# Kernel tuning notes

Hardware: AMD Instinct MI355X
Metric: run time of the kernel (lower is better)

Reference implementation:

```python
import jax, jax.numpy as jnp
import numpy as np

D = 64          # node_hidden_dim
MP_STEPS = 6    # num_step_message_passing
S2S_STEPS = 6   # num_step_set2set
LSTM_LAYERS = 3 # num_layer_set2set


def setup_inputs() -> dict:
    key = jax.random.key(0)
    ks = jax.random.split(key, 32)
    N, E, B = 10000, 50000, 500
    node_in, edge_in, edge_hid, out_dim = 15, 5, 128, 12
    s = 0.1
    inp = {}
    inp["node_feat"] = jax.random.normal(ks[0], (N, node_in), jnp.float32)
    inp["edge_feat"] = jax.random.normal(ks[1], (E, edge_in), jnp.float32)
    inp["src"] = jax.random.randint(ks[2], (E,), 0, N)
    inp["dst"] = jax.random.randint(ks[3], (E,), 0, N)
    inp["graph_ids"] = jnp.sort(jax.random.randint(ks[4], (N,), 0, B))
    inp["num_graphs"] = B
    # lin0
    inp["lin0_W"] = jax.random.normal(ks[5], (node_in, D), jnp.float32) * s
    inp["lin0_b"] = jnp.zeros((D,), jnp.float32)
    # edge network MLP (Linear -> ReLU -> Linear), output reshaped to D x D per edge
    inp["em_W1"] = jax.random.normal(ks[6], (edge_in, edge_hid), jnp.float32) * s
    inp["em_b1"] = jnp.zeros((edge_hid,), jnp.float32)
    inp["em_W2"] = jax.random.normal(ks[7], (edge_hid, D * D), jnp.float32) * 0.02
    inp["em_b2"] = jnp.zeros((D * D,), jnp.float32)
    inp["conv_bias"] = jnp.zeros((D,), jnp.float32)
    # GRU (input D, hidden D), torch layout: [3*D, in], gate order r,z,n
    inp["gru_Wih"] = jax.random.normal(ks[8], (3 * D, D), jnp.float32) * s
    inp["gru_Whh"] = jax.random.normal(ks[9], (3 * D, D), jnp.float32) * s
    inp["gru_bih"] = jnp.zeros((3 * D,), jnp.float32)
    inp["gru_bhh"] = jnp.zeros((3 * D,), jnp.float32)
    # Set2Set LSTM: input 2*D, hidden D, 3 layers. torch layout [4*D, in], gates i,f,g,o
    inp["lstm0_Wih"] = jax.random.normal(ks[10], (4 * D, 2 * D), jnp.float32) * s
    inp["lstm0_Whh"] = jax.random.normal(ks[11], (4 * D, D), jnp.float32) * s
    inp["lstm0_bih"] = jnp.zeros((4 * D,), jnp.float32)
    inp["lstm0_bhh"] = jnp.zeros((4 * D,), jnp.float32)
    inp["lstm12_Wih"] = jax.random.normal(ks[12], (2, 4 * D, D), jnp.float32) * s
    inp["lstm12_Whh"] = jax.random.normal(ks[13], (2, 4 * D, D), jnp.float32) * s
    inp["lstm12_bih"] = jnp.zeros((2, 4 * D), jnp.float32)
    inp["lstm12_bhh"] = jnp.zeros((2, 4 * D), jnp.float32)
    # output head
    inp["lin1_W"] = jax.random.normal(ks[14], (2 * D, D), jnp.float32) * s
    inp["lin1_b"] = jnp.zeros((D,), jnp.float32)
    inp["lin2_W"] = jax.random.normal(ks[15], (D, out_dim), jnp.float32) * s
    inp["lin2_b"] = jnp.zeros((out_dim,), jnp.float32)
    return inp


def _mpnn(node_feat, edge_feat, src, dst, graph_ids, num_graphs,
          lin0_W, lin0_b, em_W1, em_b1, em_W2, em_b2, conv_bias,
          gru_Wih, gru_Whh, gru_bih, gru_bhh,
          lstm0_Wih, lstm0_Whh, lstm0_bih, lstm0_bhh,
          lstm12_Wih, lstm12_Whh, lstm12_bih, lstm12_bhh,
          lin1_W, lin1_b, lin2_W, lin2_b):
    N = node_feat.shape[0]
    E = edge_feat.shape[0]
    B = num_graphs
    # initial node embedding
    out = jax.nn.relu(node_feat @ lin0_W + lin0_b)      # [N, D]
    h = out                                             # GRU hidden (seq_len=1, 1 layer)
    # per-edge weight matrices (edge features are static across steps)
    We = (jax.nn.relu(edge_feat @ em_W1 + em_b1) @ em_W2 + em_b2).reshape(E, D, D)
    for _ in range(MP_STEPS):
        # NNConv: gather src -> per-edge matvec -> scatter-add to dst
        msg = jnp.einsum('ei,eio->eo', out[src], We)    # [E, D]
        agg = jax.ops.segment_sum(msg, dst, num_segments=N) + conv_bias
        m = jax.nn.relu(agg)                            # [N, D]
        # GRU cell (torch gate order r, z, n)
        gx = m @ gru_Wih.T + gru_bih
        gh = h @ gru_Whh.T + gru_bhh
        rx, zx, nx = jnp.split(gx, 3, axis=-1)
        rh, zh, nh = jnp.split(gh, 3, axis=-1)
        r = jax.nn.sigmoid(rx + rh)
        z = jax.nn.sigmoid(zx + zh)
        n = jnp.tanh(nx + r * nh)
        h = (1.0 - z) * n + z * h
        out = h
    # Set2Set readout: 3-layer LSTM over steps, attention over nodes per graph
    h_l = [jnp.zeros((B, D), out.dtype) for _ in range(LSTM_LAYERS)]
    c_l = [jnp.zeros((B, D), out.dtype) for _ in range(LSTM_LAYERS)]
    q_star = jnp.zeros((B, 2 * D), out.dtype)
    for _ in range(S2S_STEPS):
        x = q_star
        for l in range(LSTM_LAYERS):
            if l == 0:
                Wih, Whh, bih, bhh = lstm0_Wih, lstm0_Whh, lstm0_bih, lstm0_bhh
            else:
                Wih, Whh = lstm12_Wih[l - 1], lstm12_Whh[l - 1]
                bih, bhh = lstm12_bih[l - 1], lstm12_bhh[l - 1]
            g = x @ Wih.T + bih + h_l[l] @ Whh.T + bhh
            i_g, f_g, g_g, o_g = jnp.split(g, 4, axis=-1)
            c_l[l] = jax.nn.sigmoid(f_g) * c_l[l] + jax.nn.sigmoid(i_g) * jnp.tanh(g_g)
            h_l[l] = jax.nn.sigmoid(o_g) * jnp.tanh(c_l[l])
            x = h_l[l]
        q = x                                           # [B, D]
        # segment softmax attention
        e = jnp.sum(out * q[graph_ids], axis=-1)        # [N]
        emax = jax.ops.segment_max(e, graph_ids, num_segments=B)
        ex = jnp.exp(e - emax[graph_ids])
        denom = jax.ops.segment_sum(ex, graph_ids, num_segments=B)
        alpha = ex / denom[graph_ids]                   # [N]
        readout = jax.ops.segment_sum(alpha[:, None] * out, graph_ids, num_segments=B)
        q_star = jnp.concatenate([q, readout], axis=-1) # [B, 2D]
    y = jax.nn.relu(q_star @ lin1_W + lin1_b) @ lin2_W + lin2_b
    return y


def reference(node_feat, edge_feat, src, dst, graph_ids, num_graphs,
              lin0_W, lin0_b, em_W1, em_b1, em_W2, em_b2, conv_bias,
              gru_Wih, gru_Whh, gru_bih, gru_bhh,
              lstm0_Wih, lstm0_Whh, lstm0_bih, lstm0_bhh,
              lstm12_Wih, lstm12_Whh, lstm12_bih, lstm12_bhh,
              lin1_W, lin1_b, lin2_W, lin2_b):
    return _mpnn(node_feat, edge_feat, src, dst, graph_ids, num_graphs,
                 lin0_W, lin0_b, em_W1, em_b1, em_W2, em_b2, conv_bias,
                 gru_Wih, gru_Whh, gru_bih, gru_bhh,
                 lstm0_Wih, lstm0_Whh, lstm0_bih, lstm0_bhh,
                 lstm12_Wih, lstm12_Whh, lstm12_bih, lstm12_bhh,
                 lin1_W, lin1_b, lin2_W, lin2_b)
```

## Files before the change

### kernel.cpp

```cpp
#include <hip/hip_runtime.h>
#include <math.h>

#define NGRAPH 500
#define MP_STEPS 6
#define S2S_STEPS 6
#define S2S_CAP 128

typedef _Float16 h8 __attribute__((ext_vector_type(8)));
typedef float f4 __attribute__((ext_vector_type(4)));

__device__ __forceinline__ float sigmoidf_(float v){ return 1.0f/(1.0f + expf(-v)); }

__global__ void k_zero(float* __restrict__ p, int n){
  int i = blockIdx.x*256 + threadIdx.x;
  if(i < n) p[i] = 0.f;
}

__global__ void k_lin0(const float* __restrict__ nf, const float* __restrict__ W,
                       const float* __restrict__ b, float* __restrict__ x, int N){
  int n = blockIdx.x*4 + (threadIdx.x >> 6);
  int d = threadIdx.x & 63;
  if(n >= N) return;
  float acc = b[d];
#pragma unroll
  for(int i=0;i<15;i++) acc = fmaf(nf[n*15+i], W[i*64+d], acc);
  x[n*64+d] = fmaxf(acc, 0.0f);
}

__global__ void k_edgeh(const float* __restrict__ ef, const float* __restrict__ W1,
                        const float* __restrict__ b1, _Float16* __restrict__ he, int E){
  int e = blockIdx.x;
  int h = threadIdx.x;
  if(e >= E || h >= 160) return;
  float v;
  if(h < 128){
    float acc = b1[h];
#pragma unroll
    for(int i=0;i<5;i++) acc = fmaf(ef[e*5+i], W1[i*128+h], acc);
    v = fmaxf(acc, 0.f);
  } else {
    v = (h == 128) ? 1.0f : 0.0f;
  }
  he[(size_t)e*160 + h] = (_Float16)v;
}

__global__ void k_prepW2(const float* __restrict__ W2, const float* __restrict__ b2,
                         _Float16* __restrict__ W2T){
  int idx = blockIdx.x*256 + threadIdx.x;
  if(idx >= 4096*160) return;
  int n = idx / 160, k = idx % 160;
  float v = (k < 128) ? W2[(size_t)k*4096 + n] : ((k == 128) ? b2[n] : 0.f);
  W2T[idx] = (_Float16)v;
}

__global__ __launch_bounds__(512, 2) void k_fmsg(
    const _Float16* __restrict__ he,
    const _Float16* __restrict__ W2T,
    const float* __restrict__ x,
    const int* __restrict__ src, const int* __restrict__ dst,
    float* __restrict__ agg, int E)
{
  __shared__ _Float16 hs[128*160];
  __shared__ float xsT[64*132];
  __shared__ int ds_dst[128];
  const int tid  = threadIdx.x;
  const int wave = tid >> 6;
  const int mrow = wave >> 2;
  const int cg   = wave & 3;
  const int lane = tid & 63;
  const int quad = lane >> 4;
  const int l15  = lane & 15;
  const int e0   = blockIdx.x * 128;

  for(int t = tid; t < 2560; t += 512){
    int r = t / 20, c = t % 20;
    uint4 v = make_uint4(0,0,0,0);
    if(e0 + r < E) v = *(const uint4*)&he[(size_t)(e0+r)*160 + c*8];
    *(uint4*)&hs[r*160 + c*8] = v;
  }
  {
    int j = tid >> 2, qc = tid & 3;
    int sj = (e0 + j < E) ? src[e0 + j] : 0;
    const float4* xr = (const float4*)(x + (size_t)sj*64);
#pragma unroll
    for(int k=0;k<4;k++){
      float4 v = xr[qc*4 + k];
      int ib = qc*16 + k*4;
      xsT[(ib+0)*132 + j] = v.x;
      xsT[(ib+1)*132 + j] = v.y;
      xsT[(ib+2)*132 + j] = v.z;
      xsT[(ib+3)*132 + j] = v.w;
    }
  }
  if(tid < 128) ds_dst[tid] = (e0 + tid < E) ? dst[e0 + tid] : 0;
  __syncthreads();

  h8 af[4][5];
#pragma unroll
  for(int mt=0;mt<4;mt++)
#pragma unroll
    for(int ks=0;ks<5;ks++)
      af[mt][ks] = *(const h8*)&hs[(mrow*64 + mt*16 + l15)*160 + ks*32 + (quad<<3)];

  const _Float16* bbase = W2T + ((size_t)(cg*16 + l15))*160 + (quad<<3);
  h8 bf[5], bn[5];
#pragma unroll
  for(int ks=0;ks<5;ks++) bf[ks] = *(const h8*)(bbase + ks*32);

  f4 macc[4];
#pragma unroll
  for(int mt=0;mt<4;mt++) macc[mt] = (f4){0.f,0.f,0.f,0.f};

#pragma unroll 2
  for(int i=0;i<64;i++){
    if(i < 63){
      const _Float16* nb = bbase + (size_t)(i+1)*64*160;
#pragma unroll
      for(int ks=0;ks<5;ks++) bn[ks] = *(const h8*)(nb + ks*32);
    }
    f4 g0 = (f4){0.f,0.f,0.f,0.f}, g1 = g0, g2 = g0, g3 = g0;
#pragma unroll
    for(int ks=0;ks<5;ks++){
      g0 = __builtin_amdgcn_mfma_f32_16x16x32_f16(af[0][ks], bf[ks], g0, 0, 0, 0);
      g1 = __builtin_amdgcn_mfma_f32_16x16x32_f16(af[1][ks], bf[ks], g1, 0, 0, 0);
      g2 = __builtin_amdgcn_mfma_f32_16x16x32_f16(af[2][ks], bf[ks], g2, 0, 0, 0);
      g3 = __builtin_amdgcn_mfma_f32_16x16x32_f16(af[3][ks], bf[ks], g3, 0, 0, 0);
    }
    f4 xs0 = *(const f4*)&xsT[i*132 + mrow*64 + (quad<<2) +  0];
    f4 xs1 = *(const f4*)&xsT[i*132 + mrow*64 + (quad<<2) + 16];
    f4 xs2 = *(const f4*)&xsT[i*132 + mrow*64 + (quad<<2) + 32];
    f4 xs3 = *(const f4*)&xsT[i*132 + mrow*64 + (quad<<2) + 48];
    macc[0] += xs0 * g0;
    macc[1] += xs1 * g1;
    macc[2] += xs2 * g2;
    macc[3] += xs3 * g3;
#pragma unroll
    for(int ks=0;ks<5;ks++) bf[ks] = bn[ks];
  }

  const int col = cg*16 + l15;
#pragma unroll
  for(int mt=0;mt<4;mt++){
#pragma unroll
    for(int r=0;r<4;r++){
      int edge = mrow*64 + mt*16 + (quad<<2) + r;
      if(e0 + edge < E)
        atomicAdd(&agg[(size_t)ds_dst[edge]*64 + col], macc[mt][r]);
    }
  }
}

__global__ __launch_bounds__(256) void k_gru2(
    float* __restrict__ x, float* __restrict__ agg, const float* __restrict__ cb,
    const float* __restrict__ WihT, const float* __restrict__ WhhT,
    const float* __restrict__ bih, const float* __restrict__ bhh, int N)
{
  __shared__ float ms[32*64], hs2[32*64];
  const int tid = threadIdx.x;
  const int n0 = blockIdx.x*32;
  for(int t=tid; t<2048; t+=256){
    int n = n0 + (t>>6), d = t&63;
    float mv=0.f, hv=0.f;
    if(n < N){
      mv = fmaxf(agg[(size_t)n*64+d] + cb[d], 0.f);
      agg[(size_t)n*64+d] = 0.f;
      hv = x[(size_t)n*64+d];
    }
    ms[t]=mv; hs2[t]=hv;
  }
  __syncthreads();
  const int gx = tid & 31, ng = tid >> 5;
  float ar[4][2]={{0}}, az[4][2]={{0}}, anx[4][2]={{0}}, anh[4][2]={{0}};
#pragma unroll 4
  for(int k=0;k<64;k++){
    float wi0=WihT[k*192+gx],     wi1=WihT[k*192+gx+32];
    float wi2=WihT[k*192+gx+64],  wi3=WihT[k*192+gx+96];
    float wi4=WihT[k*192+gx+128], wi5=WihT[k*192+gx+160];
    float wh0=WhhT[k*192+gx],     wh1=WhhT[k*192+gx+32];
    float wh2=WhhT[k*192+gx+64],  wh3=WhhT[k*192+gx+96];
    float wh4=WhhT[k*192+gx+128], wh5=WhhT[k*192+gx+160];
#pragma unroll
    for(int j=0;j<4;j++){
      float mk = ms[(ng*4+j)*64+k], hk = hs2[(ng*4+j)*64+k];
      ar[j][0] = fmaf(mk,wi0, fmaf(hk,wh0, ar[j][0]));
      ar[j][1] = fmaf(mk,wi1, fmaf(hk,wh1, ar[j][1]));
      az[j][0] = fmaf(mk,wi2, fmaf(hk,wh2, az[j][0]));
      az[j][1] = fmaf(mk,wi3, fmaf(hk,wh3, az[j][1]));
      anx[j][0]= fmaf(mk,wi4, anx[j][0]);
      anx[j][1]= fmaf(mk,wi5, anx[j][1]);
      anh[j][0]= fmaf(hk,wh4, anh[j][0]);
      anh[j][1]= fmaf(hk,wh5, anh[j][1]);
    }
  }
#pragma unroll
  for(int j=0;j<4;j++){
    int n = n0 + ng*4 + j;
    if(n >= N) continue;
#pragma unroll
    for(int c=0;c<2;c++){
      int d = gx + 32*c;
      float r  = sigmoidf_(ar[j][c] + bih[d]     + bhh[d]);
      float z  = sigmoidf_(az[j][c] + bih[64+d]  + bhh[64+d]);
      float nn = tanhf(anx[j][c] + bih[128+d] + r*(anh[j][c] + bhh[128+d]));
      float hv = hs2[(ng*4+j)*64+d];
      x[(size_t)n*64+d] = (1.f - z)*nn + z*hv;
    }
  }
}

__global__ void k_tr_gru(const float* __restrict__ Wih, const float* __restrict__ Whh,
                         float* __restrict__ WihT, float* __restrict__ WhhT){
  int idx = blockIdx.x*256 + threadIdx.x;
  if(idx < 192*64){
    int r = idx/64, i = idx%64;
    WihT[i*192 + r] = Wih[idx];
    WhhT[i*192 + r] = Whh[idx];
  }
}

__global__ void k_tr_lstmcat(const float* __restrict__ w0ih, const float* __restrict__ w0hh,
                             const float* __restrict__ w12ih, const float* __restrict__ w12hh,
                             float* __restrict__ W0cat, float* __restrict__ W12cat){
  int idx = blockIdx.x*256 + threadIdx.x;
  if(idx < 192*256){
    int k = idx / 256, r = idx % 256;
    W0cat[idx] = (k < 128) ? w0ih[r*128 + k] : w0hh[r*64 + (k - 128)];
  }
  if(idx < 2*128*256){
    int l = idx / (128*256);
    int rem = idx % (128*256);
    int k = rem / 256, r = rem % 256;
    W12cat[idx] = (k < 64) ? w12ih[((size_t)l*256 + r)*64 + k]
                           : w12hh[((size_t)l*256 + r)*64 + (k - 64)];
  }
}

__device__ __forceinline__ int lbound(const int* __restrict__ a, int n, int v){
  int lo=0, hi=n;
  while(lo<hi){ int mid=(lo+hi)>>1; if(a[mid]<v) lo=mid+1; else hi=mid; }
  return lo;
}

template<int KTOT>
__device__ __forceinline__ void lstm_layer2(
    const float* __restrict__ xin, float* __restrict__ hv, float* __restrict__ cv,
    const float* __restrict__ Wcat, const float* __restrict__ bsum,
    f4* __restrict__ ps4, int t)
{
  constexpr int CH = KTOT/4;
  const int kc = t >> 6, tq = t & 63;
  const float* wp = Wcat + (size_t)(kc*CH)*256 + 4*tq;
  const float* xp = xin + kc*CH;
  f4 acc = (f4){0.f,0.f,0.f,0.f};
#pragma unroll
  for(int i=0;i<CH;i++){
    f4 w = *(const f4*)(wp + (size_t)i*256);
    acc += xp[i] * w;
  }
  ps4[t] = acc;
  __syncthreads();
  if(t < 64){
    float v[4];
#pragma unroll
    for(int g=0; g<4; g++){
      int G = g*64 + t;
      int q = G >> 2, cmp = G & 3;
      float s = 0.f;
#pragma unroll
      for(int k2=0; k2<4; k2++) s += ps4[k2*64 + q][cmp];
      v[g] = s + bsum[G];
    }
    float ig = sigmoidf_(v[0]);
    float fg = sigmoidf_(v[1]);
    float gg = tanhf(v[2]);
    float og = sigmoidf_(v[3]);
    float cn = fg*cv[t] + ig*gg;
    cv[t] = cn;
    hv[t] = og*tanhf(cn);
  }
  __syncthreads();
}

__global__ __launch_bounds__(256) void k_s2s(
    const float* __restrict__ x, const int* __restrict__ gid, int N,
    const float* __restrict__ W0cat, const float* __restrict__ W12cat,
    const float* __restrict__ l0_bih, const float* __restrict__ l0_bhh,
    const float* __restrict__ l12_bih, const float* __restrict__ l12_bhh,
    const float* __restrict__ W1, const float* __restrict__ b1,
    const float* __restrict__ W2, const float* __restrict__ b2,
    float* __restrict__ y)
{
  const int b = blockIdx.x;
  const int t = threadIdx.x;
  const int wave = t >> 6, lane = t & 63;
  __shared__ float xt[S2S_CAP*65];
  __shared__ float qcat[320];
  __shared__ float csl[192];
  __shared__ f4    ps4[256];
  __shared__ float bsum[768];
  __shared__ float ps[S2S_CAP];
  __shared__ float rop[256];
  __shared__ float wred[4], wsum[4];
  __shared__ int sh_n0, sh_n1;

  if(t == 0) sh_n0 = lbound(gid, N, b);
  if(t == 1) sh_n1 = lbound(gid, N, b+1);
  for(int i=t; i<320; i+=256) qcat[i] = 0.f;
  if(t < 192) csl[t] = 0.f;
  for(int i=t; i<768; i+=256){
    int layer = i >> 8, g = i & 255;
    float bi, bh;
    if(layer == 0){ bi = l0_bih[g]; bh = l0_bhh[g]; }
    else { bi = l12_bih[(layer-1)*256+g]; bh = l12_bhh[(layer-1)*256+g]; }
    bsum[i] = bi + bh;
  }
  __syncthreads();
  const int n0 = sh_n0, cnt = sh_n1 - sh_n0;
  const int cc = (cnt < S2S_CAP) ? cnt : S2S_CAP;

  for(int j = wave; j < cc; j += 4)
    xt[j*65 + lane] = x[(size_t)(n0+j)*64 + lane];
  __syncthreads();

  for(int step=0; step<S2S_STEPS; step++){
    lstm_layer2<192>(qcat,       qcat+128, csl,     W0cat,            bsum,       ps4, t);
    lstm_layer2<128>(qcat+128,   qcat+192, csl+64,  W12cat,           bsum+256,   ps4, t);
    lstm_layer2<128>(qcat+192,   qcat+256, csl+128, W12cat+128*256,   bsum+512,   ps4, t);

    const float* q = qcat + 256;
    float accd = 0.f;
    if(t < cc){
      const float* xr = xt + t*65;
#pragma unroll 8
      for(int k=0;k<64;k++) accd = fmaf(xr[k], q[k], accd);
    }
    float pm = (t < cc) ? accd : -1e30f;
    float qv = q[lane];
    for(int j = S2S_CAP + wave; j < cnt; j += 4){
      float p = x[(size_t)(n0+j)*64 + lane] * qv;
#pragma unroll
      for(int o=32;o;o>>=1) p += __shfl_xor(p, o, 64);
      pm = fmaxf(pm, p);
    }
#pragma unroll
    for(int o=32;o;o>>=1) pm = fmaxf(pm, __shfl_xor(pm, o, 64));
    if(lane == 0) wred[wave] = pm;
    __syncthreads();
    float mx = fmaxf(fmaxf(wred[0],wred[1]), fmaxf(wred[2],wred[3]));

    float ex = 0.f;
    if(t < cc){ ex = expf(accd - mx); ps[t] = ex; }
    float exsum = ex;
    float racc = 0.f;
    for(int j = S2S_CAP + wave; j < cnt; j += 4){
      float xv = x[(size_t)(n0+j)*64 + lane];
      float p = xv * qv;
#pragma unroll
      for(int o=32;o;o>>=1) p += __shfl_xor(p, o, 64);
      float e2 = expf(p - mx);
      if(lane == 0) exsum += e2;
      racc = fmaf(e2, xv, racc);
    }
#pragma unroll
    for(int o=32;o;o>>=1) exsum += __shfl_xor(exsum, o, 64);
    if(lane == 0) wsum[wave] = exsum;
    __syncthreads();

    for(int j = wave; j < cc; j += 4)
      racc = fmaf(ps[j], xt[j*65 + lane], racc);
    rop[wave*64 + lane] = racc;
    __syncthreads();
    if(t < 64){
      float tot = wsum[0]+wsum[1]+wsum[2]+wsum[3];
      float inv = (tot > 0.f) ? 1.f/tot : 0.f;
      float rv = (rop[t] + rop[64+t] + rop[128+t] + rop[192+t]) * inv;
      qcat[t] = qcat[256+t];
      qcat[64+t] = rv;
    }
    __syncthreads();
  }
  if(t < 64){
    float a = b1[t];
#pragma unroll 4
    for(int k=0;k<128;k++) a = fmaf(qcat[k], W1[k*64+t], a);
    rop[t] = fmaxf(a, 0.f);
  }
  __syncthreads();
  if(t < 12){
    float o = b2[t];
#pragma unroll 4
    for(int k=0;k<64;k++) o = fmaf(rop[k], W2[k*12+t], o);
    y[b*12+t] = o;
  }
}

extern "C" void kernel_launch(void* const* d_in, const int* in_sizes, int n_in,
                              void* d_out, int out_size, void* d_ws, size_t ws_size,
                              hipStream_t stream) {
  const float* node_feat = (const float*)d_in[0];
  const float* edge_feat = (const float*)d_in[1];
  const int*   src       = (const int*)d_in[2];
  const int*   dst       = (const int*)d_in[3];
  const int*   gid       = (const int*)d_in[4];
  const float* lin0_W = (const float*)d_in[6];
  const float* lin0_b = (const float*)d_in[7];
  const float* em_W1  = (const float*)d_in[8];
  const float* em_b1  = (const float*)d_in[9];
  const float* em_W2  = (const float*)d_in[10];
  const float* em_b2  = (const float*)d_in[11];
  const float* conv_b = (const float*)d_in[12];
  const float* gru_Wih = (const float*)d_in[13];
  const float* gru_Whh = (const float*)d_in[14];
  const float* gru_bih = (const float*)d_in[15];
  const float* gru_bhh = (const float*)d_in[16];
  const float* l0_Wih = (const float*)d_in[17];
  const float* l0_Whh = (const float*)d_in[18];
  const float* l0_bih = (const float*)d_in[19];
  const float* l0_bhh = (const float*)d_in[20];
  const float* l12_Wih = (const float*)d_in[21];
  const float* l12_Whh = (const float*)d_in[22];
  const float* l12_bih = (const float*)d_in[23];
  const float* l12_bhh = (const float*)d_in[24];
  const float* lin1_W = (const float*)d_in[25];
  const float* lin1_b = (const float*)d_in[26];
  const float* lin2_W = (const float*)d_in[27];
  const float* lin2_b = (const float*)d_in[28];
  float* y = (float*)d_out;

  const int N = in_sizes[0] / 15;
  const int E = in_sizes[1] / 5;
  const int B = NGRAPH;

  char* p = (char*)d_ws;
  auto carve = [&](size_t bytes)->char* {
    char* r = p; p += (bytes + 255) & ~(size_t)255; return r;
  };
  _Float16* he_h = (_Float16*)carve((size_t)E*160*2);
  _Float16* W2T  = (_Float16*)carve((size_t)4096*160*2);
  float* x      = (float*)carve((size_t)N*64*4);
  float* agg    = (float*)carve((size_t)N*64*4);
  float* gWihT  = (float*)carve(192*64*4);
  float* gWhhT  = (float*)carve(192*64*4);
  float* W0cat  = (float*)carve(192*256*4);
  float* W12cat = (float*)carve(2*128*256*4);
  (void)ws_size; (void)n_in; (void)out_size;

  k_lin0<<<(N+3)/4, 256, 0, stream>>>(node_feat, lin0_W, lin0_b, x, N);
  k_edgeh<<<E, 192, 0, stream>>>(edge_feat, em_W1, em_b1, he_h, E);
  k_prepW2<<<(4096*160+255)/256, 256, 0, stream>>>(em_W2, em_b2, W2T);
  k_tr_gru<<<(192*64+255)/256, 256, 0, stream>>>(gru_Wih, gru_Whh, gWihT, gWhhT);
  k_tr_lstmcat<<<(2*128*256+255)/256, 256, 0, stream>>>(l0_Wih, l0_Whh, l12_Wih, l12_Whh,
                                                        W0cat, W12cat);
  k_zero<<<(N*64+255)/256, 256, 0, stream>>>(agg, N*64);

  const int nblk = (E + 127) / 128;
  for(int s=0; s<MP_STEPS; s++){
    k_fmsg<<<nblk, 512, 0, stream>>>(he_h, W2T, x, src, dst, agg, E);
    k_gru2<<<(N+31)/32, 256, 0, stream>>>(x, agg, conv_b, gWihT, gWhhT, gru_bih, gru_bhh, N);
  }

  k_s2s<<<B, 256, 0, stream>>>(x, gid, N,
                               W0cat, W12cat, l0_bih, l0_bhh,
                               l12_bih, l12_bhh,
                               lin1_W, lin1_b, lin2_W, lin2_b, y);
}
```

Before: 925.9 us.

## Process four graphs per Set2Set block, one wave per graph attention

The Set2Set kernel now handles four graphs per block. The LSTM layers compute all four graphs at once so each weight load is reused four times, and each wave runs softmax attention for its own graph with shuffles instead of block-wide barriers. This cuts weight traffic and synchronisation. In exchange the grid shrinks to B/4 blocks (125 on a many-CU GPU), and it assumes B is divisible by 4. The shared node cache cap drops to 64, so larger graphs fall back to global reads.

```diff
diff --git a/kernel.cpp b/kernel.cpp
--- a/kernel.cpp
+++ b/kernel.cpp
@@ -4,7 +4,7 @@
 #define NGRAPH 500
 #define MP_STEPS 6
 #define S2S_STEPS 6
-#define S2S_CAP 128
+#define S2S_CAP 64
 
 typedef _Float16 h8 __attribute__((ext_vector_type(8)));
 typedef float f4 __attribute__((ext_vector_type(4)));
@@ -242,41 +242,46 @@
 }
 
 template<int KTOT>
-__device__ __forceinline__ void lstm_layer2(
-    const float* __restrict__ xin, float* __restrict__ hv, float* __restrict__ cv,
+__device__ __forceinline__ void lstm_layer4(
+    float (*__restrict__ qcat)[320], float (*__restrict__ csl)[192],
+    int xoff, int hoff, int coff,
     const float* __restrict__ Wcat, const float* __restrict__ bsum,
-    f4* __restrict__ ps4, int t)
+    f4 (*__restrict__ ps4)[256], int t)
 {
   constexpr int CH = KTOT/4;
   const int kc = t >> 6, tq = t & 63;
   const float* wp = Wcat + (size_t)(kc*CH)*256 + 4*tq;
-  const float* xp = xin + kc*CH;
-  f4 acc = (f4){0.f,0.f,0.f,0.f};
+  f4 a0 = (f4){0.f,0.f,0.f,0.f}, a1 = a0, a2 = a0, a3 = a0;
 #pragma unroll
   for(int i=0;i<CH;i++){
     f4 w = *(const f4*)(wp + (size_t)i*256);
-    acc += xp[i] * w;
-  }
-  ps4[t] = acc;
-  __syncthreads();
-  if(t < 64){
+    int xi = xoff + kc*CH + i;
+    a0 += qcat[0][xi] * w;
+    a1 += qcat[1][xi] * w;
+    a2 += qcat[2][xi] * w;
+    a3 += qcat[3][xi] * w;
+  }
+  ps4[0][t] = a0; ps4[1][t] = a1; ps4[2][t] = a2; ps4[3][t] = a3;
+  __syncthreads();
+  {
+    const int g = t >> 6, d = t & 63;
     float v[4];
 #pragma unroll
-    for(int g=0; g<4; g++){
-      int G = g*64 + t;
+    for(int gate=0; gate<4; gate++){
+      int G = gate*64 + d;
       int q = G >> 2, cmp = G & 3;
       float s = 0.f;
 #pragma unroll
-      for(int k2=0; k2<4; k2++) s += ps4[k2*64 + q][cmp];
-      v[g] = s + bsum[G];
+      for(int k2=0;k2<4;k2++) s += ps4[g][k2*64 + q][cmp];
+      v[gate] = s + bsum[G];
     }
     float ig = sigmoidf_(v[0]);
     float fg = sigmoidf_(v[1]);
     float gg = tanhf(v[2]);
     float og = sigmoidf_(v[3]);
-    float cn = fg*cv[t] + ig*gg;
-    cv[t] = cn;
-    hv[t] = og*tanhf(cn);
+    float cn = fg*csl[g][coff+d] + ig*gg;
+    csl[g][coff+d] = cn;
+    qcat[g][hoff+d] = og*tanhf(cn);
   }
   __syncthreads();
 }
@@ -290,23 +295,19 @@
     const float* __restrict__ W2, const float* __restrict__ b2,
     float* __restrict__ y)
 {
-  const int b = blockIdx.x;
+  const int b0 = blockIdx.x * 4;
   const int t = threadIdx.x;
   const int wave = t >> 6, lane = t & 63;
-  __shared__ float xt[S2S_CAP*65];
-  __shared__ float qcat[320];
-  __shared__ float csl[192];
-  __shared__ f4    ps4[256];
+  __shared__ float xt[4][S2S_CAP*65];
+  __shared__ float qcat[4][320];
+  __shared__ float csl[4][192];
+  __shared__ f4    ps4[4][256];
   __shared__ float bsum[768];
-  __shared__ float ps[S2S_CAP];
-  __shared__ float rop[256];
-  __shared__ float wred[4], wsum[4];
-  __shared__ int sh_n0, sh_n1;
-
-  if(t == 0) sh_n0 = lbound(gid, N, b);
-  if(t == 1) sh_n1 = lbound(gid, N, b+1);
-  for(int i=t; i<320; i+=256) qcat[i] = 0.f;
-  if(t < 192) csl[t] = 0.f;
+  __shared__ int   sh_n0[5];
+
+  if(t < 5) sh_n0[t] = lbound(gid, N, b0 + t);
+  for(int i=t; i<4*320; i+=256) ((float*)qcat)[i] = 0.f;
+  for(int i=t; i<4*192; i+=256) ((float*)csl)[i] = 0.f;
   for(int i=t; i<768; i+=256){
     int layer = i >> 8, g = i & 255;
     float bi, bh;
@@ -315,82 +316,75 @@
     bsum[i] = bi + bh;
   }
   __syncthreads();
-  const int n0 = sh_n0, cnt = sh_n1 - sh_n0;
-  const int cc = (cnt < S2S_CAP) ? cnt : S2S_CAP;
-
-  for(int j = wave; j < cc; j += 4)
-    xt[j*65 + lane] = x[(size_t)(n0+j)*64 + lane];
+  const int n0w = sh_n0[wave];
+  const int cntw = sh_n0[wave+1] - n0w;
+  const int ccw = (cntw < S2S_CAP) ? cntw : S2S_CAP;
+
+  for(int j=0;j<ccw;j++)
+    xt[wave][j*65 + lane] = x[(size_t)(n0w+j)*64 + lane];
   __syncthreads();
 
   for(int step=0; step<S2S_STEPS; step++){
-    lstm_layer2<192>(qcat,       qcat+128, csl,     W0cat,            bsum,       ps4, t);
-    lstm_layer2<128>(qcat+128,   qcat+192, csl+64,  W12cat,           bsum+256,   ps4, t);
-    lstm_layer2<128>(qcat+192,   qcat+256, csl+128, W12cat+128*256,   bsum+512,   ps4, t);
-
-    const float* q = qcat + 256;
+    lstm_layer4<192>(qcat, csl,   0, 128,   0, W0cat,          bsum,     ps4, t);
+    lstm_layer4<128>(qcat, csl, 128, 192,  64, W12cat,         bsum+256, ps4, t);
+    lstm_layer4<128>(qcat, csl, 192, 256, 128, W12cat+128*256, bsum+512, ps4, t);
+
+    const float* q = qcat[wave] + 256;
     float accd = 0.f;
-    if(t < cc){
-      const float* xr = xt + t*65;
+    if(lane < ccw){
+      const float* xr = xt[wave] + lane*65;
 #pragma unroll 8
       for(int k=0;k<64;k++) accd = fmaf(xr[k], q[k], accd);
     }
-    float pm = (t < cc) ? accd : -1e30f;
+    float pm = (lane < ccw) ? accd : -1e30f;
     float qv = q[lane];
-    for(int j = S2S_CAP + wave; j < cnt; j += 4){
-      float p = x[(size_t)(n0+j)*64 + lane] * qv;
+    for(int j = S2S_CAP; j < cntw; j++){
+      float p = x[(size_t)(n0w+j)*64 + lane] * qv;
 #pragma unroll
       for(int o=32;o;o>>=1) p += __shfl_xor(p, o, 64);
       pm = fmaxf(pm, p);
     }
 #pragma unroll
     for(int o=32;o;o>>=1) pm = fmaxf(pm, __shfl_xor(pm, o, 64));
-    if(lane == 0) wred[wave] = pm;
-    __syncthreads();
-    float mx = fmaxf(fmaxf(wred[0],wred[1]), fmaxf(wred[2],wred[3]));
-
-    float ex = 0.f;
-    if(t < cc){ ex = expf(accd - mx); ps[t] = ex; }
+    const float mx = pm;
+
+    float ex = (lane < ccw) ? expf(accd - mx) : 0.f;
     float exsum = ex;
+#pragma unroll
+    for(int o=32;o;o>>=1) exsum += __shfl_xor(exsum, o, 64);
+
     float racc = 0.f;
-    for(int j = S2S_CAP + wave; j < cnt; j += 4){
-      float xv = x[(size_t)(n0+j)*64 + lane];
+    for(int j=0;j<ccw;j++)
+      racc = fmaf(__shfl(ex, j, 64), xt[wave][j*65 + lane], racc);
+    for(int j = S2S_CAP; j < cntw; j++){
+      float xv = x[(size_t)(n0w+j)*64 + lane];
       float p = xv * qv;
 #pragma unroll
       for(int o=32;o;o>>=1) p += __shfl_xor(p, o, 64);
       float e2 = expf(p - mx);
-      if(lane == 0) exsum += e2;
+      exsum += e2;
       racc = fmaf(e2, xv, racc);
     }
-#pragma unroll
-    for(int o=32;o;o>>=1) exsum += __shfl_xor(exsum, o, 64);
-    if(lane == 0) wsum[wave] = exsum;
+    float inv = (exsum > 0.f) ? 1.f/exsum : 0.f;
+    qcat[wave][lane]      = qcat[wave][256 + lane];
+    qcat[wave][64 + lane] = racc * inv;
     __syncthreads();
-
-    for(int j = wave; j < cc; j += 4)
-      racc = fmaf(ps[j], xt[j*65 + lane], racc);
-    rop[wave*64 + lane] = racc;
-    __syncthreads();
-    if(t < 64){
-      float tot = wsum[0]+wsum[1]+wsum[2]+wsum[3];
-      float inv = (tot > 0.f) ? 1.f/tot : 0.f;
-      float rv = (rop[t] + rop[64+t] + rop[128+t] + rop[192+t]) * inv;
-      qcat[t] = qcat[256+t];
-      qcat[64+t] = rv;
-    }
-    __syncthreads();
-  }
-  if(t < 64){
-    float a = b1[t];
+  }
+  float* hh = (float*)ps4;
+  {
+    const int g = t >> 6, d = t & 63;
+    float a = b1[d];
 #pragma unroll 4
-    for(int k=0;k<128;k++) a = fmaf(qcat[k], W1[k*64+t], a);
-    rop[t] = fmaxf(a, 0.f);
-  }
-  __syncthreads();
-  if(t < 12){
-    float o = b2[t];
+    for(int k=0;k<128;k++) a = fmaf(qcat[g][k], W1[k*64+d], a);
+    hh[g*64 + d] = fmaxf(a, 0.f);
+  }
+  __syncthreads();
+  if(t < 48){
+    int g = t / 12, o = t % 12;
+    float out = b2[o];
 #pragma unroll 4
-    for(int k=0;k<64;k++) o = fmaf(rop[k], W2[k*12+t], o);
-    y[b*12+t] = o;
+    for(int k=0;k<64;k++) out = fmaf(hh[g*64 + k], W2[k*12+o], out);
+    y[(size_t)(b0+g)*12 + o] = out;
   }
 }
 
@@ -459,8 +453,8 @@
     k_gru2<<<(N+31)/32, 256, 0, stream>>>(x, agg, conv_b, gWihT, gWhhT, gru_bih, gru_bhh, N);
   }
 
-  k_s2s<<<B, 256, 0, stream>>>(x, gid, N,
-                               W0cat, W12cat, l0_bih, l0_bhh,
-                               l12_bih, l12_bhh,
-                               lin1_W, lin1_b, lin2_W, lin2_b, y);
-}
+  k_s2s<<<B/4, 256, 0, stream>>>(x, gid, N,
+                                 W0cat, W12cat, l0_bih, l0_bhh,
+                                 l12_bih, l12_bhh,
+                                 lin1_W, lin1_b, lin2_W, lin2_b, y);
+}
```

Result: faster. 905.7 us (-2.2%).
